# Kernel optimization log

Hardware: AMD Instinct MI355X
Metric: run time of the kernel (lower is better)

## Reference

```python
import jax, jax.numpy as jnp
import numpy as np

N = 100000
E = 1600000
F_IN = 128
F_HID = 128
BN_EPS = 1e-5


def setup_inputs() -> dict:
    key = jax.random.key(0)
    ks = jax.random.split(key, 10)
    x = jax.random.normal(ks[0], (N, F_IN), dtype=jnp.float32)
    edge_index = jax.random.randint(ks[1], (2, E), 0, N, dtype=jnp.int64)
    s = 1.0 / np.sqrt(F_IN)
    w0 = jax.random.uniform(ks[2], (F_IN, F_HID), jnp.float32, -s, s)
    b0 = jax.random.uniform(ks[3], (F_HID,), jnp.float32, -s, s)
    gamma = jnp.ones((F_HID,), jnp.float32)
    beta = jnp.zeros((F_HID,), jnp.float32)
    rmean = 0.1 * jax.random.normal(ks[4], (F_HID,), jnp.float32)
    rvar = 0.5 + jax.random.uniform(ks[5], (F_HID,), jnp.float32)
    s2 = 1.0 / np.sqrt(F_HID)
    w1 = jax.random.uniform(ks[6], (F_HID, F_HID), jnp.float32, -s2, s2)
    b1 = jax.random.uniform(ks[7], (F_HID,), jnp.float32, -s2, s2)
    return {"x": x, "edge_index": edge_index, "w0": w0, "b0": b0,
            "gamma": gamma, "beta": beta, "rmean": rmean, "rvar": rvar,
            "w1": w1, "b1": b1}


def _gin_conv(x, src, dst, w, b):
    # GINConv with eps=0: Linear(x + sum_{j->i} x_j)
    agg = jax.ops.segment_sum(x[src], dst, num_segments=N)
    return (x + agg) @ w + b


def reference(x, edge_index, w0, b0, gamma, beta, rmean, rvar, w1, b1):
    src = edge_index[0]
    dst = edge_index[1]
    h = _gin_conv(x, src, dst, w0, b0)
    # BatchNorm1d in eval mode (running stats), then ReLU; dropout is identity.
    h = gamma * (h - rmean) * jax.lax.rsqrt(rvar + BN_EPS) + beta
    h = jax.nn.relu(h)
    out = _gin_conv(h, src, dst, w1, b1)
    return out
```

## Files before the change

### kernel.cpp

```cpp
#include <hip/hip_runtime.h>
#include <cstddef>

#define NN 100000
#define EE 1600000
#define FF 128
#define NCHUNK ((NN + 255) / 256)

typedef unsigned int uint;
typedef unsigned short ushort;
typedef short short8 __attribute__((ext_vector_type(8)));
typedef float f32x4 __attribute__((ext_vector_type(4)));

__device__ __forceinline__ ushort f2bf(float f) {
  uint u = __float_as_uint(f);
  uint r = u + 0x7fffu + ((u >> 16) & 1u);
  return (ushort)(r >> 16);
}
__device__ __forceinline__ uint pack2(float a, float b) {
  return (uint)f2bf(a) | ((uint)f2bf(b) << 16);
}
__device__ __forceinline__ void acc8(float* a, uint4 v) {
  a[0] += __uint_as_float(v.x << 16);
  a[1] += __uint_as_float(v.x & 0xffff0000u);
  a[2] += __uint_as_float(v.y << 16);
  a[3] += __uint_as_float(v.y & 0xffff0000u);
  a[4] += __uint_as_float(v.z << 16);
  a[5] += __uint_as_float(v.z & 0xffff0000u);
  a[6] += __uint_as_float(v.w << 16);
  a[7] += __uint_as_float(v.w & 0xffff0000u);
}

__global__ __launch_bounds__(256) void cvt_bf16(const float4* __restrict__ x,
                                                uint4* __restrict__ xb, int n8) {
  int i = blockIdx.x * 256 + threadIdx.x;
  if (i >= n8) return;
  float4 a = x[2 * i];
  float4 b = x[2 * i + 1];
  uint4 o;
  o.x = pack2(a.x, a.y);
  o.y = pack2(a.z, a.w);
  o.z = pack2(b.x, b.y);
  o.w = pack2(b.z, b.w);
  xb[i] = o;
}

__global__ __launch_bounds__(256) void cvt_wt(const float* __restrict__ w,
                                              ushort* __restrict__ wt) {
  int i = blockIdx.x * 256 + threadIdx.x;
  int k = i >> 7, n = i & 127;
  wt[n * FF + k] = f2bf(w[(size_t)k * FF + n]);
}

__global__ __launch_bounds__(256) void hist(const int* __restrict__ ei,
                                            int* __restrict__ counts) {
  int e = blockIdx.x * 256 + threadIdx.x;
  if (e < EE) atomicAdd(&counts[ei[EE + e]], 1);
}

__global__ __launch_bounds__(256) void scan_chunks(const int* __restrict__ counts,
                                                   int* __restrict__ incl,
                                                   int* __restrict__ chunkSum) {
  __shared__ int sd[256];
  int i = blockIdx.x * 256 + threadIdx.x;
  sd[threadIdx.x] = (i < NN) ? counts[i] : 0;
  __syncthreads();
  for (int off = 1; off < 256; off <<= 1) {
    int t = 0;
    if ((int)threadIdx.x >= off) t = sd[threadIdx.x - off];
    __syncthreads();
    if ((int)threadIdx.x >= off) sd[threadIdx.x] += t;
    __syncthreads();
  }
  if (i < NN) incl[i] = sd[threadIdx.x];
  if (threadIdx.x == 255) chunkSum[blockIdx.x] = sd[255];
}

__global__ __launch_bounds__(512) void scan_sums(int* __restrict__ chunkSum) {
  __shared__ int sd[512];
  sd[threadIdx.x] = (threadIdx.x < NCHUNK) ? chunkSum[threadIdx.x] : 0;
  __syncthreads();
  for (int off = 1; off < 512; off <<= 1) {
    int t = 0;
    if ((int)threadIdx.x >= off) t = sd[threadIdx.x - off];
    __syncthreads();
    if ((int)threadIdx.x >= off) sd[threadIdx.x] += t;
    __syncthreads();
  }
  if (threadIdx.x < NCHUNK) chunkSum[threadIdx.x] = sd[threadIdx.x];
}

__global__ __launch_bounds__(256) void finalize(const int* __restrict__ counts,
                                                const int* __restrict__ incl,
                                                const int* __restrict__ chunkSum,
                                                int* __restrict__ offsets,
                                                int* __restrict__ cursor) {
  int i = blockIdx.x * 256 + threadIdx.x;
  if (i < NN) {
    int base = (blockIdx.x > 0) ? chunkSum[blockIdx.x - 1] : 0;
    int off = base + incl[i] - counts[i];
    offsets[i] = off;
    cursor[i] = off;
  }
  if (i == 0) offsets[NN] = EE;
}

__global__ __launch_bounds__(256) void fill(const int* __restrict__ ei,
                                            int* __restrict__ cursor,
                                            int* __restrict__ csr) {
  int e = blockIdx.x * 256 + threadIdx.x;
  if (e < EE) {
    int p = atomicAdd(&cursor[ei[EE + e]], 1);
    csr[p] = ei[e];
  }
}

__global__ __launch_bounds__(256) void gather_bf16(const uint4* __restrict__ feat,
                                                   const int* __restrict__ offsets,
                                                   const int* __restrict__ csr,
                                                   ushort* __restrict__ out) {
  int t = blockIdx.x * 256 + threadIdx.x;
  int g = t >> 4;
  int l = t & 15;
  if (g >= NN) return;
  int beg = offsets[g];
  int end = offsets[g + 1];
  float acc[8] = {};
  acc8(acc, feat[(size_t)g * 16 + l]);
  int j = beg;
  for (; j + 4 <= end; j += 4) {
    int i0 = csr[j], i1 = csr[j + 1], i2 = csr[j + 2], i3 = csr[j + 3];
    uint4 v0 = feat[(size_t)i0 * 16 + l];
    uint4 v1 = feat[(size_t)i1 * 16 + l];
    uint4 v2 = feat[(size_t)i2 * 16 + l];
    uint4 v3 = feat[(size_t)i3 * 16 + l];
    acc8(acc, v0); acc8(acc, v1); acc8(acc, v2); acc8(acc, v3);
  }
  for (; j < end; ++j) acc8(acc, feat[(size_t)csr[j] * 16 + l]);
  uint4 o;
  o.x = pack2(acc[0], acc[1]);
  o.y = pack2(acc[2], acc[3]);
  o.z = pack2(acc[4], acc[5]);
  o.w = pack2(acc[6], acc[7]);
  ((uint4*)(out + (size_t)g * FF))[l] = o;
}

template <bool BN, bool OUT16>
__global__ __launch_bounds__(256) void gemm_mfma(const ushort* __restrict__ a,
    const ushort* __restrict__ bt, const float* __restrict__ bias,
    const float* __restrict__ gamma, const float* __restrict__ beta,
    const float* __restrict__ rmean, const float* __restrict__ rvar,
    void* __restrict__ out0, int nrows)
{
  const int tid = threadIdx.x;
  const int wv = tid >> 6;
  const int l = tid & 63;
  const int lane16 = l & 15;
  const int quad = l >> 4;
  const int rowbase = blockIdx.x * 128 + wv * 32;

  f32x4 acc[2][8] = {};

  for (int kc = 0; kc < FF; kc += 32) {
    short8 af[2];
#pragma unroll
    for (int rt = 0; rt < 2; ++rt) {
      int r = min(rowbase + rt * 16 + lane16, nrows - 1);
      af[rt] = *(const short8*)(a + (size_t)r * FF + kc + quad * 8);
    }
#pragma unroll
    for (int ct = 0; ct < 8; ++ct) {
      int n = ct * 16 + lane16;
      short8 bf = *(const short8*)(bt + n * FF + kc + quad * 8);
      acc[0][ct] = __builtin_amdgcn_mfma_f32_16x16x32_bf16(af[0], bf, acc[0][ct], 0, 0, 0);
      acc[1][ct] = __builtin_amdgcn_mfma_f32_16x16x32_bf16(af[1], bf, acc[1][ct], 0, 0, 0);
    }
  }

  float sc[8], sh[8];
#pragma unroll
  for (int ct = 0; ct < 8; ++ct) {
    int c = ct * 16 + lane16;
    if (BN) {
      float s = gamma[c] * rsqrtf(rvar[c] + 1e-5f);
      sc[ct] = s;
      sh[ct] = (bias[c] - rmean[c]) * s + beta[c];
    } else {
      sc[ct] = 1.0f;
      sh[ct] = bias[c];
    }
  }

#pragma unroll
  for (int rt = 0; rt < 2; ++rt) {
#pragma unroll
    for (int reg = 0; reg < 4; ++reg) {
      int r = rowbase + rt * 16 + quad * 4 + reg;
      if (r < nrows) {
#pragma unroll
        for (int ct = 0; ct < 8; ++ct) {
          int c = ct * 16 + lane16;
          float v = fmaf(acc[rt][ct][reg], sc[ct], sh[ct]);
          if (BN) v = fmaxf(v, 0.0f);
          if (OUT16) ((ushort*)out0)[(size_t)r * FF + c] = f2bf(v);
          else       ((float*)out0)[(size_t)r * FF + c] = v;
        }
      }
    }
  }
}

extern "C" void kernel_launch(void* const* d_in, const int* in_sizes, int n_in,
                              void* d_out, int out_size, void* d_ws, size_t ws_size,
                              hipStream_t stream) {
  const float* x     = (const float*)d_in[0];
  const int*   ei    = (const int*)d_in[1];
  const float* w0    = (const float*)d_in[2];
  const float* b0    = (const float*)d_in[3];
  const float* gamma = (const float*)d_in[4];
  const float* beta  = (const float*)d_in[5];
  const float* rmean = (const float*)d_in[6];
  const float* rvar  = (const float*)d_in[7];
  const float* w1    = (const float*)d_in[8];
  const float* b1    = (const float*)d_in[9];
  float* out = (float*)d_out;

  ushort* sb  = (ushort*)d_ws;
  ushort* xb  = sb + (size_t)NN * FF;
  ushort* hb  = xb + (size_t)NN * FF;
  ushort* wt0 = hb + (size_t)NN * FF;
  ushort* wt1 = wt0 + FF * FF;
  int* counts   = (int*)(wt1 + FF * FF);
  int* incl     = counts + NN;
  int* chunkSum = incl + NN;
  int* offsets  = chunkSum + 512;
  int* cursor   = offsets + NN + 1;
  int* csr      = cursor + NN;

  const int eb = (EE + 255) / 256;
  const int cvb = (NN * FF / 8 + 255) / 256;
  const int gatherb = (NN * 16 + 255) / 256;
  const int gemmb = (NN + 127) / 128;

  (void)hipMemsetAsync(counts, 0, (size_t)NN * sizeof(int), stream);
  hist<<<eb, 256, 0, stream>>>(ei, counts);
  scan_chunks<<<NCHUNK, 256, 0, stream>>>(counts, incl, chunkSum);
  scan_sums<<<1, 512, 0, stream>>>(chunkSum);
  finalize<<<NCHUNK, 256, 0, stream>>>(counts, incl, chunkSum, offsets, cursor);
  fill<<<eb, 256, 0, stream>>>(ei, cursor, csr);

  cvt_bf16<<<cvb, 256, 0, stream>>>((const float4*)x, (uint4*)xb, NN * FF / 8);
  cvt_wt<<<64, 256, 0, stream>>>(w0, wt0);
  cvt_wt<<<64, 256, 0, stream>>>(w1, wt1);

  gather_bf16<<<gatherb, 256, 0, stream>>>((const uint4*)xb, offsets, csr, sb);
  gemm_mfma<true, true><<<gemmb, 256, 0, stream>>>(sb, wt0, b0, gamma, beta,
                                                   rmean, rvar, (void*)hb, NN);
  gather_bf16<<<gatherb, 256, 0, stream>>>((const uint4*)hb, offsets, csr, sb);
  gemm_mfma<false, false><<<gemmb, 256, 0, stream>>>(sb, wt1, b1, nullptr, nullptr,
                                                     nullptr, nullptr, (void*)out, NN);
}
```

Measured before the change: 485.1 us.

## Build CSR via two-pass bucketed scatter with shared-memory atomics

Replaces the single global-atomic CSR fill with a two-level binning scheme. Edges are first grouped by destination bucket of 512 nodes, using per-block shared-memory histograms and scans, and written contiguously into a pairs buffer. A second kernel then places each bucket's edges into the CSR using shared-memory cursors. This removes the random global atomics on a per-node cursor array, at the cost of an extra pass over an 8-byte-per-edge intermediate buffer and two extra launches.

```diff
diff --git a/kernel.cpp b/kernel.cpp
--- a/kernel.cpp
+++ b/kernel.cpp
@@ -5,6 +5,9 @@
 #define EE 1600000
 #define FF 128
 #define NCHUNK ((NN + 255) / 256)
+#define BSH 9
+#define NB ((NN + 511) / 512)
+#define EPB 4096
 
 typedef unsigned int uint;
 typedef unsigned short ushort;
@@ -92,25 +95,106 @@
 __global__ __launch_bounds__(256) void finalize(const int* __restrict__ counts,
                                                 const int* __restrict__ incl,
                                                 const int* __restrict__ chunkSum,
-                                                int* __restrict__ offsets,
-                                                int* __restrict__ cursor) {
+                                                int* __restrict__ offsets) {
   int i = blockIdx.x * 256 + threadIdx.x;
   if (i < NN) {
     int base = (blockIdx.x > 0) ? chunkSum[blockIdx.x - 1] : 0;
-    int off = base + incl[i] - counts[i];
-    offsets[i] = off;
-    cursor[i] = off;
+    offsets[i] = base + incl[i] - counts[i];
   }
   if (i == 0) offsets[NN] = EE;
 }
 
-__global__ __launch_bounds__(256) void fill(const int* __restrict__ ei,
-                                            int* __restrict__ cursor,
-                                            int* __restrict__ csr) {
-  int e = blockIdx.x * 256 + threadIdx.x;
-  if (e < EE) {
-    int p = atomicAdd(&cursor[ei[EE + e]], 1);
-    csr[p] = ei[e];
+__global__ __launch_bounds__(256) void init_bcur(const int* __restrict__ chunkSum,
+                                                 int* __restrict__ bcur) {
+  int b = blockIdx.x * 256 + threadIdx.x;
+  if (b < NB) bcur[b] = b ? chunkSum[2 * b - 1] : 0;
+}
+
+__global__ __launch_bounds__(256) void binscatter(const int* __restrict__ ei,
+                                                  int* __restrict__ bcur,
+                                                  uint2* __restrict__ pairs) {
+  __shared__ uint2 lpair[EPB];
+  __shared__ int hcnt[256];
+  __shared__ int hincl[256];
+  __shared__ int hbase[256];
+  const int t = threadIdx.x;
+  const int e0 = blockIdx.x * EPB;
+
+  hcnt[t] = 0;
+  __syncthreads();
+
+  int es[16], ed[16];
+#pragma unroll
+  for (int i = 0; i < 16; ++i) {
+    int e = e0 + t + i * 256;
+    if (e < EE) {
+      es[i] = ei[e];
+      ed[i] = ei[EE + e];
+      atomicAdd(&hcnt[ed[i] >> BSH], 1);
+    } else {
+      es[i] = -1;
+      ed[i] = 0;
+    }
+  }
+  __syncthreads();
+
+  const int mycnt = hcnt[t];
+  hincl[t] = mycnt;
+  __syncthreads();
+  for (int off = 1; off < 256; off <<= 1) {
+    int tv = 0;
+    if (t >= off) tv = hincl[t - off];
+    __syncthreads();
+    if (t >= off) hincl[t] += tv;
+    __syncthreads();
+  }
+  if (t < NB && mycnt > 0) hbase[t] = atomicAdd(&bcur[t], mycnt);
+  const int lbase = hincl[t] - mycnt;
+  __syncthreads();
+  hcnt[t] = lbase;
+  __syncthreads();
+
+#pragma unroll
+  for (int i = 0; i < 16; ++i) {
+    if (es[i] >= 0) {
+      int b = ed[i] >> BSH;
+      int pos = atomicAdd(&hcnt[b], 1);
+      lpair[pos] = make_uint2((uint)es[i], (uint)ed[i]);
+    }
+  }
+  __syncthreads();
+
+  const int total = hincl[255];
+  for (int i = t; i < total; i += 256) {
+    int lo = 0, hi = 255;
+    while (lo < hi) {
+      int mid = (lo + hi) >> 1;
+      if (hincl[mid] > i) hi = mid; else lo = mid + 1;
+    }
+    int b = lo;
+    int lb = b ? hincl[b - 1] : 0;
+    pairs[(size_t)hbase[b] + (i - lb)] = lpair[i];
+  }
+}
+
+__global__ __launch_bounds__(256) void fill2(const uint2* __restrict__ pairs,
+                                             const int* __restrict__ offsets,
+                                             int* __restrict__ csr) {
+  __shared__ int cur[512];
+  const int t = threadIdx.x;
+  const int v0 = blockIdx.x << BSH;
+  const int v1 = min(v0 + 512, NN);
+  for (int i = t; i < 512; i += 256) {
+    int v = v0 + i;
+    cur[i] = (v < NN) ? offsets[v] : 0;
+  }
+  __syncthreads();
+  const int pbeg = offsets[v0];
+  const int pend = offsets[v1];
+  for (int j = pbeg + t; j < pend; j += 256) {
+    uint2 p = pairs[j];
+    int pos = atomicAdd(&cur[(int)p.y - v0], 1);
+    csr[pos] = (int)p.x;
   }
 }
 
@@ -229,24 +313,28 @@
   ushort* hb  = xb + (size_t)NN * FF;
   ushort* wt0 = hb + (size_t)NN * FF;
   ushort* wt1 = wt0 + FF * FF;
-  int* counts   = (int*)(wt1 + FF * FF);
+  uint2* pairs  = (uint2*)(wt1 + FF * FF);
+  int* csr      = (int*)(pairs + (size_t)EE);
+  int* counts   = csr + EE;
   int* incl     = counts + NN;
   int* chunkSum = incl + NN;
   int* offsets  = chunkSum + 512;
-  int* cursor   = offsets + NN + 1;
-  int* csr      = cursor + NN;
+  int* bcur     = offsets + NN + 1;
 
   const int eb = (EE + 255) / 256;
   const int cvb = (NN * FF / 8 + 255) / 256;
   const int gatherb = (NN * 16 + 255) / 256;
   const int gemmb = (NN + 127) / 128;
+  const int binb = (EE + EPB - 1) / EPB;
 
   (void)hipMemsetAsync(counts, 0, (size_t)NN * sizeof(int), stream);
   hist<<<eb, 256, 0, stream>>>(ei, counts);
   scan_chunks<<<NCHUNK, 256, 0, stream>>>(counts, incl, chunkSum);
   scan_sums<<<1, 512, 0, stream>>>(chunkSum);
-  finalize<<<NCHUNK, 256, 0, stream>>>(counts, incl, chunkSum, offsets, cursor);
-  fill<<<eb, 256, 0, stream>>>(ei, cursor, csr);
+  finalize<<<NCHUNK, 256, 0, stream>>>(counts, incl, chunkSum, offsets);
+  init_bcur<<<1, 256, 0, stream>>>(chunkSum, bcur);
+  binscatter<<<binb, 256, 0, stream>>>(ei, bcur, pairs);
+  fill2<<<NB, 256, 0, stream>>>(pairs, offsets, csr);
 
   cvt_bf16<<<cvb, 256, 0, stream>>>((const float4*)x, (uint4*)xb, NN * FF / 8);
   cvt_wt<<<64, 256, 0, stream>>>(w0, wt0);
```

New measurement: 415.2 us. 14.4% less time.
